# Performance work log

Measured on AMD Instinct MI355X. Metric: run time of the kernel, lower is better.

## Reference

```python
import jax, jax.numpy as jnp
import numpy as np

N, E, G = 200000, 800000, 8192
IN, H, D, EXTRA = 128, 4, 64, 16


def setup_inputs() -> dict:
    key = jax.random.key(0)
    ks = jax.random.split(key, 24)
    inp = {
        'feats_node': jax.random.normal(ks[0], (N, IN), jnp.float32),
        'feats_graph': jax.random.normal(ks[1], (G, EXTRA), jnp.float32),
        'src': jax.random.randint(ks[2], (E,), 0, N, jnp.int32),
        'dst': jax.random.randint(ks[3], (E,), 0, N, jnp.int32),
        'graph_ids': jnp.sort(jax.random.randint(ks[4], (N,), 0, G, jnp.int32)),
        # GAT layer 1: fc [H*D, IN], attn [H, D], bias zeros (DGL default)
        'fc1_w': 0.5 * jax.random.normal(ks[5], (H * D, IN), jnp.float32),
        'attn_l1': 0.5 * jax.random.normal(ks[6], (H, D), jnp.float32),
        'attn_r1': 0.5 * jax.random.normal(ks[7], (H, D), jnp.float32),
        'bias1': jnp.zeros((H * D,), jnp.float32),
        # GAT layer 2
        'fc2_w': 0.5 * jax.random.normal(ks[8], (H * D, H * D), jnp.float32),
        'attn_l2': 0.5 * jax.random.normal(ks[9], (H, D), jnp.float32),
        'attn_r2': 0.5 * jax.random.normal(ks[10], (H, D), jnp.float32),
        'bias2': jnp.zeros((H * D,), jnp.float32),
        # GAT layer 3: 1 head
        'fc3_w': 0.5 * jax.random.normal(ks[11], (D, H * D), jnp.float32),
        'attn_l3': 0.5 * jax.random.normal(ks[12], (1, D), jnp.float32),
        'attn_r3': 0.5 * jax.random.normal(ks[13], (1, D), jnp.float32),
        'bias3': jnp.zeros((D,), jnp.float32),
        # readout score
        'score_w': 0.5 * jax.random.normal(ks[14], (1, D), jnp.float32),
        'score_b': jnp.zeros((1,), jnp.float32),
        # MLP: [D+EXTRA -> 2D -> D -> 1]
        'mlp_w1': 0.5 * jax.random.normal(ks[15], (2 * D, D + EXTRA), jnp.float32),
        'mlp_b1': jnp.zeros((2 * D,), jnp.float32),
        'mlp_w2': 0.5 * jax.random.normal(ks[16], (D, 2 * D), jnp.float32),
        'mlp_b2': jnp.zeros((D,), jnp.float32),
        'mlp_w3': 0.5 * jax.random.normal(ks[17], (1, D), jnp.float32),
        'mlp_b3': jnp.zeros((1,), jnp.float32),
    }
    return inp


def gat_conv(x, src, dst, fc_w, attn_l, attn_r, bias, n_heads, out_dim):
    # DGL GATConv: proj -> edge leaky_relu attention -> per-dst softmax -> aggregate
    n = x.shape[0]
    feat = (x @ fc_w.T).reshape(n, n_heads, out_dim)          # [N,H,D]
    el = jnp.einsum('nhd,hd->nh', feat, attn_l)               # [N,H]
    er = jnp.einsum('nhd,hd->nh', feat, attn_r)
    e = jax.nn.leaky_relu(el[src] + er[dst], 0.2)             # [E,H]
    m = jax.ops.segment_max(e, dst, num_segments=n)           # per-dst max
    m = jax.lax.stop_gradient(jnp.where(jnp.isfinite(m), m, 0.0))
    a = jnp.exp(e - m[dst])                                   # [E,H]
    denom = jax.ops.segment_sum(a, dst, num_segments=n)       # [N,H]
    alpha = a / jnp.where(denom[dst] == 0, 1.0, denom[dst])
    out = jax.ops.segment_sum(alpha[:, :, None] * feat[src], dst, num_segments=n)
    return out + bias.reshape(1, n_heads, out_dim)            # [N,H,D]


def reference(feats_node, feats_graph, src, dst, graph_ids,
              fc1_w, attn_l1, attn_r1, bias1,
              fc2_w, attn_l2, attn_r2, bias2,
              fc3_w, attn_l3, attn_r3, bias3,
              score_w, score_b,
              mlp_w1, mlp_b1, mlp_w2, mlp_b2, mlp_w3, mlp_b3):
    n = feats_node.shape[0]
    g = feats_graph.shape[0]
    x = jax.nn.selu(gat_conv(feats_node, src, dst, fc1_w, attn_l1, attn_r1, bias1, H, D)).reshape(n, H * D)
    x = jax.nn.selu(gat_conv(x, src, dst, fc2_w, attn_l2, attn_r2, bias2, H, D)).reshape(n, H * D)
    x = jax.nn.selu(gat_conv(x, src, dst, fc3_w, attn_l3, attn_r3, bias3, 1, D)).reshape(n, D)
    # weighted-average readout: sum(w*x)/sum(w) per graph
    w = jax.nn.sigmoid(x @ score_w.T + score_b)               # [N,1]
    num = jax.ops.segment_sum(w * x, graph_ids, num_segments=g)
    den = jax.ops.segment_sum(w, graph_ids, num_segments=g)
    emb = num / jnp.where(den == 0, 1.0, den)                 # [G,D]
    z = jnp.concatenate([emb, feats_graph], axis=1)           # [G,D+EXTRA]
    h = jax.nn.selu(z @ mlp_w1.T + mlp_b1)
    h = jax.nn.selu(h @ mlp_w2.T + mlp_b2)
    return h @ mlp_w3.T + mlp_b3                              # [G,1]
```

## Files before the change

### kernel.cpp

```cpp
#include <hip/hip_runtime.h>
#include <math.h>

#define N_NODES 200000
#define N_EDGES 800000
#define N_GRAPHS 8192
#define B1 16
#define B2G 16
#define EC2 128

typedef unsigned short ushort_t;

__device__ __forceinline__ float selu_f(float x){
  const float alpha = 1.6732632423543772f;
  const float lam   = 1.0507009873554805f;
  return x > 0.f ? lam * x : lam * alpha * (expf(x) - 1.f);
}
__device__ __forceinline__ float dot4(float4 a, float4 b){
  return a.x * b.x + a.y * b.y + a.z * b.z + a.w * b.w;
}

__global__ void zero_i32(int* p, int n){
  int i = blockIdx.x * 256 + threadIdx.x;
  if (i < n) p[i] = 0;
}

__global__ void deg_kernel(const int* __restrict__ dst, int* __restrict__ deg, int E){
  int e = blockIdx.x * 256 + threadIdx.x;
  if (e < E) atomicAdd(&deg[dst[e]], 1);
}

__global__ void scan1(const int* __restrict__ deg, int* __restrict__ rp, int* __restrict__ bs, int n){
  __shared__ int sh[256];
  int t = threadIdx.x;
  int base = blockIdx.x * 1024;
  int v[4]; int s = 0;
  #pragma unroll
  for (int i = 0; i < 4; i++){
    int idx = base + t * 4 + i;
    v[i] = (idx < n) ? deg[idx] : 0;
    s += v[i];
  }
  sh[t] = s; __syncthreads();
  for (int off = 1; off < 256; off <<= 1){
    int x = (t >= off) ? sh[t - off] : 0;
    __syncthreads();
    sh[t] += x;
    __syncthreads();
  }
  int run = (t == 0) ? 0 : sh[t - 1];
  #pragma unroll
  for (int i = 0; i < 4; i++){
    int idx = base + t * 4 + i;
    if (idx < n) rp[idx] = run;
    run += v[i];
  }
  if (t == 255) bs[blockIdx.x] = sh[255];
}

__global__ void scan2(int* bs, int nb){
  __shared__ int sh[256];
  int t = threadIdx.x;
  sh[t] = (t < nb) ? bs[t] : 0; __syncthreads();
  for (int off = 1; off < 256; off <<= 1){
    int x = (t >= off) ? sh[t - off] : 0;
    __syncthreads();
    sh[t] += x;
    __syncthreads();
  }
  int excl = (t == 0) ? 0 : sh[t - 1];
  if (t < nb) bs[t] = excl;
}

__global__ void scan3(int* rp, const int* __restrict__ bs, int n, int total){
  int i = blockIdx.x * 256 + threadIdx.x;
  if (i < n) rp[i] += bs[i >> 10];
  if (i == 0) rp[n] = total;
}

__global__ void fill_csr(const int* __restrict__ src, const int* __restrict__ dst,
                         const int* __restrict__ rp, int* __restrict__ fil,
                         int* __restrict__ csr, int E){
  int e = blockIdx.x * 256 + threadIdx.x;
  if (e < E){
    int d = dst[e];
    int p = atomicAdd(&fil[d], 1);
    csr[rp[d] + p] = src[e];
  }
}

__global__ void compute_v(const float* __restrict__ W1, const float* __restrict__ al1, const float* __restrict__ ar1,
                          const float* __restrict__ W2, const float* __restrict__ al2, const float* __restrict__ ar2,
                          const float* __restrict__ W3, const float* __restrict__ al3, const float* __restrict__ ar3,
                          float* __restrict__ V1L, float* __restrict__ V1R,
                          float* __restrict__ V2L, float* __restrict__ V2R,
                          float* __restrict__ V3L, float* __restrict__ V3R){
  int i = blockIdx.x * 256 + threadIdx.x;
  if (i < 512){
    int h = i >> 7, k = i & 127;
    float sl = 0.f, sr = 0.f;
    for (int dd = 0; dd < 64; dd++){
      float w = W1[(size_t)(h * 64 + dd) * 128 + k];
      sl += al1[h * 64 + dd] * w;
      sr += ar1[h * 64 + dd] * w;
    }
    V1L[i] = sl; V1R[i] = sr;
  } else if (i < 1536){
    int j = i - 512;
    int h = j >> 8, k = j & 255;
    float sl = 0.f, sr = 0.f;
    for (int dd = 0; dd < 64; dd++){
      float w = W2[(size_t)(h * 64 + dd) * 256 + k];
      sl += al2[h * 64 + dd] * w;
      sr += ar2[h * 64 + dd] * w;
    }
    V2L[j] = sl; V2R[j] = sr;
  } else if (i < 1792){
    int k = i - 1536;
    float sl = 0.f, sr = 0.f;
    for (int dd = 0; dd < 64; dd++){
      float w = W3[(size_t)dd * 256 + k];
      sl += al3[dd] * w;
      sr += ar3[dd] * w;
    }
    V3L[k] = sl; V3R[k] = sr;
  }
}

__global__ __launch_bounds__(256) void el_er1(const float* __restrict__ x0,
                                              const float* __restrict__ V1L, const float* __restrict__ V1R,
                                              float* __restrict__ el1, float* __restrict__ er1, int n){
  __shared__ float vl[512], vr[512];
  int t = threadIdx.x;
  for (int i = t; i < 512; i += 256){ vl[i] = V1L[i]; vr[i] = V1R[i]; }
  __syncthreads();
  int node = blockIdx.x * 4 + (t >> 6);
  int l = t & 63;
  if (node >= n) return;
  float xa = x0[(size_t)node * 128 + l];
  float xb = x0[(size_t)node * 128 + 64 + l];
  #pragma unroll
  for (int h = 0; h < 4; h++){
    float pl = xa * vl[h * 128 + l] + xb * vl[h * 128 + 64 + l];
    float pr = xa * vr[h * 128 + l] + xb * vr[h * 128 + 64 + l];
    #pragma unroll
    for (int off = 32; off; off >>= 1){ pl += __shfl_xor(pl, off); pr += __shfl_xor(pr, off); }
    if (l == 0){ el1[(size_t)node * 4 + h] = pl; er1[(size_t)node * 4 + h] = pr; }
  }
}

__global__ __launch_bounds__(256) void alpha_h4(const float* __restrict__ el, const float* __restrict__ er,
                                                const int* __restrict__ rp, const int* __restrict__ csr,
                                                float* __restrict__ a, int n){
  int node = blockIdx.x * 256 + threadIdx.x;
  if (node >= n) return;
  int s0 = rp[node], s1 = rp[node + 1];
  if (s0 >= s1) return;
  float4 erv = *reinterpret_cast<const float4*>(er + (size_t)node * 4);
  float m0 = -1e30f, m1 = -1e30f, m2 = -1e30f, m3 = -1e30f;
  for (int i = s0; i < s1; i++){
    float4 e = *reinterpret_cast<const float4*>(el + (size_t)csr[i] * 4);
    float e0 = e.x + erv.x; e0 = e0 > 0.f ? e0 : 0.2f * e0; m0 = fmaxf(m0, e0);
    float e1 = e.y + erv.y; e1 = e1 > 0.f ? e1 : 0.2f * e1; m1 = fmaxf(m1, e1);
    float e2 = e.z + erv.z; e2 = e2 > 0.f ? e2 : 0.2f * e2; m2 = fmaxf(m2, e2);
    float e3 = e.w + erv.w; e3 = e3 > 0.f ? e3 : 0.2f * e3; m3 = fmaxf(m3, e3);
  }
  float d0 = 0.f, d1 = 0.f, d2 = 0.f, d3 = 0.f;
  for (int i = s0; i < s1; i++){
    float4 e = *reinterpret_cast<const float4*>(el + (size_t)csr[i] * 4);
    float e0 = e.x + erv.x; e0 = e0 > 0.f ? e0 : 0.2f * e0; d0 += expf(e0 - m0);
    float e1 = e.y + erv.y; e1 = e1 > 0.f ? e1 : 0.2f * e1; d1 += expf(e1 - m1);
    float e2 = e.z + erv.z; e2 = e2 > 0.f ? e2 : 0.2f * e2; d2 += expf(e2 - m2);
    float e3 = e.w + erv.w; e3 = e3 > 0.f ? e3 : 0.2f * e3; d3 += expf(e3 - m3);
  }
  d0 = 1.f / d0; d1 = 1.f / d1; d2 = 1.f / d2; d3 = 1.f / d3;
  for (int i = s0; i < s1; i++){
    float4 e = *reinterpret_cast<const float4*>(el + (size_t)csr[i] * 4);
    float4 o;
    float e0 = e.x + erv.x; e0 = e0 > 0.f ? e0 : 0.2f * e0; o.x = expf(e0 - m0) * d0;
    float e1 = e.y + erv.y; e1 = e1 > 0.f ? e1 : 0.2f * e1; o.y = expf(e1 - m1) * d1;
    float e2 = e.z + erv.z; e2 = e2 > 0.f ? e2 : 0.2f * e2; o.z = expf(e2 - m2) * d2;
    float e3 = e.w + erv.w; e3 = e3 > 0.f ? e3 : 0.2f * e3; o.w = expf(e3 - m3) * d3;
    *reinterpret_cast<float4*>(a + (size_t)i * 4) = o;
  }
}

__global__ __launch_bounds__(256) void alpha_h1(const float* __restrict__ el, const float* __restrict__ er,
                                                const int* __restrict__ rp, const int* __restrict__ csr,
                                                float* __restrict__ a, int n){
  int node = blockIdx.x * 256 + threadIdx.x;
  if (node >= n) return;
  int s0 = rp[node], s1 = rp[node + 1];
  if (s0 >= s1) return;
  float erv = er[node];
  float m = -1e30f;
  for (int i = s0; i < s1; i++){
    float e = el[csr[i]] + erv; e = e > 0.f ? e : 0.2f * e; m = fmaxf(m, e);
  }
  float den = 0.f;
  for (int i = s0; i < s1; i++){
    float e = el[csr[i]] + erv; e = e > 0.f ? e : 0.2f * e; den += expf(e - m);
  }
  float inv = 1.f / den;
  for (int i = s0; i < s1; i++){
    float e = el[csr[i]] + erv; e = e > 0.f ? e : 0.2f * e; a[i] = expf(e - m) * inv;
  }
}

__global__ __launch_bounds__(512, 4) void l1_fused(
    const float* __restrict__ x0, const float* __restrict__ W1, const float* __restrict__ bias1,
    const float* __restrict__ a1, const float* __restrict__ W2,
    const float* __restrict__ V2L, const float* __restrict__ V2R,
    const int* __restrict__ rp, const int* __restrict__ csr,
    ushort_t* __restrict__ y1hi, unsigned char* __restrict__ y1lo,
    float* __restrict__ el2, float* __restrict__ er2){
  __shared__ float aggT[4][B1][132];
  __shared__ int rpc[B1 + 1];
  float* x1s = &aggT[0][0][0];
  int t = threadIdx.x;
  int nb0 = blockIdx.x * B1;
  if (t <= B1) rpc[t] = rp[nb0 + t];
  __syncthreads();

  {
    int g = t >> 5, c4 = t & 31;
    int i0 = rpc[g], i1 = rpc[g + 1];
    float acc[4][4] = {{0.f}};
    int s = (i0 < i1) ? csr[i0] : 0;
    for (int i = i0; i < i1; i++){
      int sn = (i + 1 < i1) ? csr[i + 1] : 0;
      float4 av = *reinterpret_cast<const float4*>(a1 + (size_t)i * 4);
      float4 xv = *reinterpret_cast<const float4*>(x0 + (size_t)s * 128 + c4 * 4);
      acc[0][0] += av.x * xv.x; acc[0][1] += av.x * xv.y; acc[0][2] += av.x * xv.z; acc[0][3] += av.x * xv.w;
      acc[1][0] += av.y * xv.x; acc[1][1] += av.y * xv.y; acc[1][2] += av.y * xv.z; acc[1][3] += av.y * xv.w;
      acc[2][0] += av.z * xv.x; acc[2][1] += av.z * xv.y; acc[2][2] += av.z * xv.z; acc[2][3] += av.z * xv.w;
      acc[3][0] += av.w * xv.x; acc[3][1] += av.w * xv.y; acc[3][2] += av.w * xv.z; acc[3][3] += av.w * xv.w;
      s = sn;
    }
    #pragma unroll
    for (int h = 0; h < 4; h++){
      float4 v = make_float4(acc[h][0], acc[h][1], acc[h][2], acc[h][3]);
      *reinterpret_cast<float4*>(&aggT[h][g][c4 * 4]) = v;
    }
  }
  __syncthreads();

  float r1[8];
  {
    int m = t & 255, dq = t >> 8;
    int h = m >> 6;
    #pragma unroll
    for (int r = 0; r < 8; r++) r1[r] = 0.f;
    const float* wp = W1 + (size_t)m * 128;
    #pragma unroll 4
    for (int kq = 0; kq < 32; kq++){
      float4 w = *reinterpret_cast<const float4*>(wp + kq * 4);
      #pragma unroll
      for (int r = 0; r < 8; r++){
        float4 a = *reinterpret_cast<const float4*>(&aggT[h][dq * 8 + r][kq * 4]);
        r1[r] += dot4(w, a);
      }
    }
  }
  __syncthreads();
  {
    int m = t & 255, dq = t >> 8;
    float b = bias1[m];
    #pragma unroll
    for (int r = 0; r < 8; r++)
      x1s[(dq * 8 + r) * 260 + m] = selu_f(r1[r] + b);
  }
  __syncthreads();

  {
    int m = t & 255, dq = t >> 8;
    float acc[8];
    #pragma unroll
    for (int r = 0; r < 8; r++) acc[r] = 0.f;
    const float* wp = W2 + (size_t)m * 256;
    #pragma unroll 4
    for (int kq = 0; kq < 64; kq++){
      float4 w = *reinterpret_cast<const float4*>(wp + kq * 4);
      #pragma unroll
      for (int r = 0; r < 8; r++){
        float4 xv = *reinterpret_cast<const float4*>(&x1s[(dq * 8 + r) * 260 + kq * 4]);
        acc[r] += dot4(w, xv);
      }
    }
    #pragma unroll
    for (int r = 0; r < 8; r++){
      int d = dq * 8 + r;
      unsigned int u = __float_as_uint(acc[r]);
      u += 0x80u;
      y1hi[(size_t)(nb0 + d) * 256 + m] = (ushort_t)(u >> 16);
      y1lo[(size_t)(nb0 + d) * 256 + m] = (unsigned char)(u >> 8);
    }
  }

  if (t < 128){
    int d = t & 15, hq = (t >> 4) & 3, lr = t >> 6;
    const float* V = lr ? V2R : V2L;
    const float4* Vq = reinterpret_cast<const float4*>(V + hq * 256);
    const float4* Xq = reinterpret_cast<const float4*>(&x1s[d * 260]);
    float p = 0.f;
    #pragma unroll 4
    for (int q = 0; q < 64; q++){
      float4 v = Vq[q]; float4 x = Xq[q];
      p += v.x * x.x; p += v.y * x.y; p += v.z * x.z; p += v.w * x.w;
    }
    if (lr) er2[(size_t)(nb0 + d) * 4 + hq] = p;
    else    el2[(size_t)(nb0 + d) * 4 + hq] = p;
  }
}

__global__ __launch_bounds__(256, 4) void l2_gather(
    const ushort_t* __restrict__ y1hi, const unsigned char* __restrict__ y1lo,
    const float* __restrict__ bias2, const float* __restrict__ a2,
    const float* __restrict__ W3,
    const float* __restrict__ V3L, const float* __restrict__ V3R,
    const int* __restrict__ rp, const int* __restrict__ csr,
    float* __restrict__ feat3, float* __restrict__ el3, float* __restrict__ er3){
  __shared__ float x2s[B2G][257];
  __shared__ float W3c[16 * 257];
  __shared__ float als[EC2][4];
  __shared__ int   ssrc[EC2];
  __shared__ int   rpc[B2G + 1];
  int t = threadIdx.x;
  int nb0 = blockIdx.x * B2G;
  if (t <= B2G) rpc[t] = rp[nb0 + t];
  __syncthreads();
  int e0 = rpc[0], eN = rpc[B2G];
  int c = t;
  int h = c >> 6;

  float acc[B2G];
  #pragma unroll
  for (int d = 0; d < B2G; d++) acc[d] = 0.f;

  for (int c0 = e0; c0 < eN; c0 += EC2){
    int ce = min(EC2, eN - c0);
    for (int i = t; i < ce; i += 256){
      ssrc[i] = csr[c0 + i];
      float4 av = *reinterpret_cast<const float4*>(a2 + (size_t)(c0 + i) * 4);
      als[i][0] = av.x; als[i][1] = av.y; als[i][2] = av.z; als[i][3] = av.w;
    }
    __syncthreads();
    #pragma unroll
    for (int d = 0; d < B2G; d++){
      int lo = max(rpc[d], c0) - c0;
      int hi = min(rpc[d + 1], c0 + ce) - c0;
      for (int i = lo; i < hi; i++){
        size_t s = (size_t)ssrc[i] * 256 + c;
        unsigned int u = ((unsigned int)y1hi[s] << 16) | ((unsigned int)y1lo[s] << 8);
        acc[d] += als[i][h] * __uint_as_float(u);
      }
    }
    __syncthreads();
  }
  {
    float b = bias2[c];
    #pragma unroll
    for (int d = 0; d < B2G; d++) x2s[d][c] = selu_f(acc[d] + b);
  }
  __syncthreads();

  {
    int task = t >> 3, j = t & 7;
    int d = task & 15, lr = task >> 4;
    const float* V = lr ? V3R : V3L;
    float p = 0.f;
    for (int kk = 0; kk < 32; kk++){
      int k = j + kk * 8;
      p += V[k] * x2s[d][k];
    }
    p += __shfl_xor(p, 1); p += __shfl_xor(p, 2); p += __shfl_xor(p, 4);
    if (j == 0){ if (lr) er3[nb0 + d] = p; else el3[nb0 + d] = p; }
  }

  for (int ch = 0; ch < 4; ch++){
    __syncthreads();
    for (int i = t; i < 16 * 64; i += 256){
      int r = i >> 6, k4 = i & 63;
      float4 w = *reinterpret_cast<const float4*>(W3 + (size_t)(ch * 16 + r) * 256 + k4 * 4);
      W3c[r * 257 + k4 * 4 + 0] = w.x; W3c[r * 257 + k4 * 4 + 1] = w.y;
      W3c[r * 257 + k4 * 4 + 2] = w.z; W3c[r * 257 + k4 * 4 + 3] = w.w;
    }
    __syncthreads();
    {
      int r = t & 15, d = t >> 4;
      float s = 0.f;
      #pragma unroll 4
      for (int k = 0; k < 256; k++) s += W3c[r * 257 + k] * x2s[d][k];
      feat3[(size_t)(nb0 + d) * 64 + ch * 16 + r] = s;
    }
  }
}

__global__ __launch_bounds__(256) void gat_agg3(const float* __restrict__ feat, const float* __restrict__ a3,
                                                const int* __restrict__ rp, const int* __restrict__ csr,
                                                const float* __restrict__ bias,
                                                float* __restrict__ out, int n){
  int node = blockIdx.x * 4 + (threadIdx.x >> 6);
  int t = threadIdx.x & 63;
  if (node >= n) return;
  int s0 = rp[node], s1 = rp[node + 1];
  float acc = 0.f;
  for (int i = s0; i < s1; i += 4){
    float a[4], f[4];
    #pragma unroll
    for (int j = 0; j < 4; j++){
      int idx = i + j;
      bool vld = idx < s1;
      int idc = vld ? idx : s1 - 1;
      float av = a3[idc];
      if (!vld) av = 0.f;
      a[j] = av;
      f[j] = feat[(size_t)csr[idc] * 64 + t];
    }
    acc += a[0] * f[0] + a[1] * f[1] + a[2] * f[2] + a[3] * f[3];
  }
  out[(size_t)node * 64 + t] = selu_f(acc + bias[t]);
}

__global__ void readout_kernel(const float* __restrict__ x3, const float* __restrict__ score_w,
                               const float* __restrict__ score_b, const int* __restrict__ gids,
                               float* __restrict__ num, float* __restrict__ den, int n){
  int node = blockIdx.x * 4 + (threadIdx.x >> 6);
  int lane = threadIdx.x & 63;
  if (node >= n) return;
  float xv = x3[(size_t)node * 64 + lane];
  float p = xv * score_w[lane];
  #pragma unroll
  for (int off = 32; off; off >>= 1) p += __shfl_xor(p, off);
  float w = 1.f / (1.f + expf(-(p + score_b[0])));
  int g = gids[node];
  atomicAdd(&num[(size_t)g * 64 + lane], w * xv);
  if (lane == 0) atomicAdd(&den[g], w);
}

__global__ __launch_bounds__(128) void mlp_kernel(
    const float* __restrict__ num, const float* __restrict__ den,
    const float* __restrict__ fg,
    const float* __restrict__ w1, const float* __restrict__ b1,
    const float* __restrict__ w2, const float* __restrict__ b2,
    const float* __restrict__ w3, const float* __restrict__ b3,
    float* __restrict__ out, int G){
  __shared__ float z[80];
  __shared__ float h1[128];
  __shared__ float h2[64];
  int t = threadIdx.x;
  for (int g = blockIdx.x; g < G; g += gridDim.x){
    if (t < 64){
      float d = den[g];
      d = (d == 0.f) ? 1.f : d;
      z[t] = num[(size_t)g * 64 + t] / d;
    } else if (t < 80){
      z[t] = fg[(size_t)g * 16 + (t - 64)];
    }
    __syncthreads();
    {
      float a = b1[t];
      for (int k = 0; k < 80; k++) a += z[k] * w1[t * 80 + k];
      h1[t] = selu_f(a);
    }
    __syncthreads();
    if (t < 64){
      float a = b2[t];
      for (int k = 0; k < 128; k++) a += h1[k] * w2[t * 128 + k];
      h2[t] = selu_f(a);
    }
    __syncthreads();
    if (t < 64){
      float p = h2[t] * w3[t];
      #pragma unroll
      for (int off = 32; off; off >>= 1) p += __shfl_down(p, off);
      if (t == 0) out[g] = p + b3[0];
    }
    __syncthreads();
  }
}

extern "C" void kernel_launch(void* const* d_in, const int* in_sizes, int n_in,
                              void* d_out, int out_size, void* d_ws, size_t ws_size,
                              hipStream_t stream) {
  const float* feats_node  = (const float*)d_in[0];
  const float* feats_graph = (const float*)d_in[1];
  const int*   src         = (const int*)d_in[2];
  const int*   dst         = (const int*)d_in[3];
  const int*   gids        = (const int*)d_in[4];
  const float* fc1_w   = (const float*)d_in[5];
  const float* attn_l1 = (const float*)d_in[6];
  const float* attn_r1 = (const float*)d_in[7];
  const float* bias1   = (const float*)d_in[8];
  const float* fc2_w   = (const float*)d_in[9];
  const float* attn_l2 = (const float*)d_in[10];
  const float* attn_r2 = (const float*)d_in[11];
  const float* bias2   = (const float*)d_in[12];
  const float* fc3_w   = (const float*)d_in[13];
  const float* attn_l3 = (const float*)d_in[14];
  const float* attn_r3 = (const float*)d_in[15];
  const float* bias3   = (const float*)d_in[16];
  const float* score_w = (const float*)d_in[17];
  const float* score_b = (const float*)d_in[18];
  const float* mlp_w1  = (const float*)d_in[19];
  const float* mlp_b1  = (const float*)d_in[20];
  const float* mlp_w2  = (const float*)d_in[21];
  const float* mlp_b2  = (const float*)d_in[22];
  const float* mlp_w3  = (const float*)d_in[23];
  const float* mlp_b3  = (const float*)d_in[24];
  float* out = (float*)d_out;

  char* ws = (char*)d_ws;
  size_t off = 0;
  auto alloc = [&](size_t bytes) -> void* {
    void* p = ws + off;
    off += (bytes + 255) / 256 * 256;
    return p;
  };
  int*   deg   = (int*)alloc((size_t)N_NODES * 4);
  int*   fil   = (int*)alloc((size_t)N_NODES * 4);
  int*   rp    = (int*)alloc((size_t)(N_NODES + 1) * 4);
  int*   bs    = (int*)alloc(256 * 4);
  int*   csr   = (int*)alloc((size_t)N_EDGES * 4);
  float* elbuf = (float*)alloc((size_t)N_NODES * 4 * 4);
  float* erbuf = (float*)alloc((size_t)N_NODES * 4 * 4);
  float* V1L   = (float*)alloc(512 * 4);
  float* V1R   = (float*)alloc(512 * 4);
  float* V2L   = (float*)alloc(1024 * 4);
  float* V2R   = (float*)alloc(1024 * 4);
  float* V3L   = (float*)alloc(256 * 4);
  float* V3R   = (float*)alloc(256 * 4);
  float* num   = (float*)alloc((size_t)N_GRAPHS * 64 * 4);
  float* den   = (float*)alloc((size_t)N_GRAPHS * 4);
  float* A     = (float*)alloc((size_t)N_EDGES * 4 * 4);
  float* feat3 = (float*)alloc((size_t)N_NODES * 64 * 4);
  ushort_t*      y1hi = (ushort_t*)alloc((size_t)N_NODES * 256 * 2);
  unsigned char* y1lo = (unsigned char*)alloc((size_t)N_NODES * 256);
  float* x3 = (float*)y1hi;

  zero_i32<<<(N_NODES + 255) / 256, 256, 0, stream>>>(deg, N_NODES);
  zero_i32<<<(N_NODES + 255) / 256, 256, 0, stream>>>(fil, N_NODES);
  zero_i32<<<(N_GRAPHS * 64 + 255) / 256, 256, 0, stream>>>((int*)num, N_GRAPHS * 64);
  zero_i32<<<(N_GRAPHS + 255) / 256, 256, 0, stream>>>((int*)den, N_GRAPHS);

  deg_kernel<<<(N_EDGES + 255) / 256, 256, 0, stream>>>(dst, deg, N_EDGES);
  scan1<<<196, 256, 0, stream>>>(deg, rp, bs, N_NODES);
  scan2<<<1, 256, 0, stream>>>(bs, 196);
  scan3<<<(N_NODES + 255) / 256, 256, 0, stream>>>(rp, bs, N_NODES, N_EDGES);
  fill_csr<<<(N_EDGES + 255) / 256, 256, 0, stream>>>(src, dst, rp, fil, csr, N_EDGES);

  compute_v<<<7, 256, 0, stream>>>(fc1_w, attn_l1, attn_r1, fc2_w, attn_l2, attn_r2,
                                   fc3_w, attn_l3, attn_r3, V1L, V1R, V2L, V2R, V3L, V3R);
  el_er1<<<N_NODES / 4, 256, 0, stream>>>(feats_node, V1L, V1R, elbuf, erbuf, N_NODES);

  alpha_h4<<<(N_NODES + 255) / 256, 256, 0, stream>>>(elbuf, erbuf, rp, csr, A, N_NODES);
  l1_fused<<<N_NODES / B1, 512, 0, stream>>>(feats_node, fc1_w, bias1, A, fc2_w,
                                             V2L, V2R, rp, csr, y1hi, y1lo, elbuf, erbuf);
  alpha_h4<<<(N_NODES + 255) / 256, 256, 0, stream>>>(elbuf, erbuf, rp, csr, A, N_NODES);
  l2_gather<<<N_NODES / B2G, 256, 0, stream>>>(y1hi, y1lo, bias2, A, fc3_w,
                                               V3L, V3R, rp, csr, feat3, elbuf, erbuf);
  alpha_h1<<<(N_NODES + 255) / 256, 256, 0, stream>>>(elbuf, erbuf, rp, csr, A, N_NODES);
  gat_agg3<<<N_NODES / 4, 256, 0, stream>>>(feat3, A, rp, csr, bias3, x3, N_NODES);

  readout_kernel<<<N_NODES / 4, 256, 0, stream>>>(x3, score_w, score_b, gids, num, den, N_NODES);
  mlp_kernel<<<256, 128, 0, stream>>>(num, den, feats_graph,
                                      mlp_w1, mlp_b1, mlp_w2, mlp_b2, mlp_w3, mlp_b3,
                                      out, N_GRAPHS);
}
```

Baseline: 2.430 ms.

## Double layer-1 node block and register-tile the fused GEMMs 4x4 per thread

Layer-1 fused kernel now processes 32 nodes per block instead of 16. The gather phase uses 16 threads per node with 8 columns each. Both dense projections (W1 and W2) now compute a 4-output by 4-node register tile per thread, so each weight load is reused across more nodes and each shared-memory read feeds four outputs. The packed hi/lo stores are vectorized. The aggT shared array is enlarged to hold x1s for 32 rows, which raises shared-memory use and register pressure and may reduce occupancy.

```diff
diff --git a/kernel.cpp b/kernel.cpp
--- a/kernel.cpp
+++ b/kernel.cpp
@@ -4,7 +4,7 @@
 #define N_NODES 200000
 #define N_EDGES 800000
 #define N_GRAPHS 8192
-#define B1 16
+#define B1 32
 #define B2G 16
 #define EC2 128
 
@@ -213,7 +213,7 @@
     const int* __restrict__ rp, const int* __restrict__ csr,
     ushort_t* __restrict__ y1hi, unsigned char* __restrict__ y1lo,
     float* __restrict__ el2, float* __restrict__ er2){
-  __shared__ float aggT[4][B1][132];
+  __shared__ float aggT[4][33][132];
   __shared__ int rpc[B1 + 1];
   float* x1s = &aggT[0][0][0];
   int t = threadIdx.x;
@@ -222,82 +222,124 @@
   __syncthreads();
 
   {
-    int g = t >> 5, c4 = t & 31;
+    int g = t >> 4, c8 = t & 15;
     int i0 = rpc[g], i1 = rpc[g + 1];
-    float acc[4][4] = {{0.f}};
+    float acc[4][8] = {{0.f}};
     int s = (i0 < i1) ? csr[i0] : 0;
     for (int i = i0; i < i1; i++){
       int sn = (i + 1 < i1) ? csr[i + 1] : 0;
       float4 av = *reinterpret_cast<const float4*>(a1 + (size_t)i * 4);
-      float4 xv = *reinterpret_cast<const float4*>(x0 + (size_t)s * 128 + c4 * 4);
-      acc[0][0] += av.x * xv.x; acc[0][1] += av.x * xv.y; acc[0][2] += av.x * xv.z; acc[0][3] += av.x * xv.w;
-      acc[1][0] += av.y * xv.x; acc[1][1] += av.y * xv.y; acc[1][2] += av.y * xv.z; acc[1][3] += av.y * xv.w;
-      acc[2][0] += av.z * xv.x; acc[2][1] += av.z * xv.y; acc[2][2] += av.z * xv.z; acc[2][3] += av.z * xv.w;
-      acc[3][0] += av.w * xv.x; acc[3][1] += av.w * xv.y; acc[3][2] += av.w * xv.z; acc[3][3] += av.w * xv.w;
+      float4 xa = *reinterpret_cast<const float4*>(x0 + (size_t)s * 128 + c8 * 8);
+      float4 xb = *reinterpret_cast<const float4*>(x0 + (size_t)s * 128 + c8 * 8 + 4);
+      acc[0][0] += av.x * xa.x; acc[0][1] += av.x * xa.y; acc[0][2] += av.x * xa.z; acc[0][3] += av.x * xa.w;
+      acc[0][4] += av.x * xb.x; acc[0][5] += av.x * xb.y; acc[0][6] += av.x * xb.z; acc[0][7] += av.x * xb.w;
+      acc[1][0] += av.y * xa.x; acc[1][1] += av.y * xa.y; acc[1][2] += av.y * xa.z; acc[1][3] += av.y * xa.w;
+      acc[1][4] += av.y * xb.x; acc[1][5] += av.y * xb.y; acc[1][6] += av.y * xb.z; acc[1][7] += av.y * xb.w;
+      acc[2][0] += av.z * xa.x; acc[2][1] += av.z * xa.y; acc[2][2] += av.z * xa.z; acc[2][3] += av.z * xa.w;
+      acc[2][4] += av.z * xb.x; acc[2][5] += av.z * xb.y; acc[2][6] += av.z * xb.z; acc[2][7] += av.z * xb.w;
+      acc[3][0] += av.w * xa.x; acc[3][1] += av.w * xa.y; acc[3][2] += av.w * xa.z; acc[3][3] += av.w * xa.w;
+      acc[3][4] += av.w * xb.x; acc[3][5] += av.w * xb.y; acc[3][6] += av.w * xb.z; acc[3][7] += av.w * xb.w;
       s = sn;
     }
     #pragma unroll
     for (int h = 0; h < 4; h++){
-      float4 v = make_float4(acc[h][0], acc[h][1], acc[h][2], acc[h][3]);
-      *reinterpret_cast<float4*>(&aggT[h][g][c4 * 4]) = v;
+      float4 v0 = make_float4(acc[h][0], acc[h][1], acc[h][2], acc[h][3]);
+      float4 v1 = make_float4(acc[h][4], acc[h][5], acc[h][6], acc[h][7]);
+      *reinterpret_cast<float4*>(&aggT[h][g][c8 * 8]) = v0;
+      *reinterpret_cast<float4*>(&aggT[h][g][c8 * 8 + 4]) = v1;
     }
   }
   __syncthreads();
 
-  float r1[8];
+  int wv = t >> 6, ln = t & 63;
+  int hh = wv & 3;
+  int mq = hh * 16 + (ln & 15);
+  int dg = (wv >> 2) * 4 + (ln >> 4);
+  int m0 = mq * 4;
+
+  float acc1[4][4];
   {
-    int m = t & 255, dq = t >> 8;
-    int h = m >> 6;
-    #pragma unroll
-    for (int r = 0; r < 8; r++) r1[r] = 0.f;
-    const float* wp = W1 + (size_t)m * 128;
-    #pragma unroll 4
+    #pragma unroll
+    for (int j = 0; j < 4; j++)
+      #pragma unroll
+      for (int r = 0; r < 4; r++) acc1[j][r] = 0.f;
+    const float* wp = W1 + (size_t)m0 * 128;
+    #pragma unroll 2
     for (int kq = 0; kq < 32; kq++){
-      float4 w = *reinterpret_cast<const float4*>(wp + kq * 4);
+      int k = kq * 4;
+      float4 w0 = *reinterpret_cast<const float4*>(wp + k);
+      float4 w1 = *reinterpret_cast<const float4*>(wp + 128 + k);
+      float4 w2 = *reinterpret_cast<const float4*>(wp + 256 + k);
+      float4 w3 = *reinterpret_cast<const float4*>(wp + 384 + k);
       #pragma unroll
-      for (int r = 0; r < 8; r++){
-        float4 a = *reinterpret_cast<const float4*>(&aggT[h][dq * 8 + r][kq * 4]);
-        r1[r] += dot4(w, a);
+      for (int r = 0; r < 4; r++){
+        float4 a = *reinterpret_cast<const float4*>(&aggT[hh][dg + 8 * r][k]);
+        acc1[0][r] += dot4(w0, a);
+        acc1[1][r] += dot4(w1, a);
+        acc1[2][r] += dot4(w2, a);
+        acc1[3][r] += dot4(w3, a);
       }
     }
   }
   __syncthreads();
   {
-    int m = t & 255, dq = t >> 8;
-    float b = bias1[m];
-    #pragma unroll
-    for (int r = 0; r < 8; r++)
-      x1s[(dq * 8 + r) * 260 + m] = selu_f(r1[r] + b);
+    float4 b = *reinterpret_cast<const float4*>(bias1 + m0);
+    #pragma unroll
+    for (int r = 0; r < 4; r++){
+      int d = dg + 8 * r;
+      float4 v;
+      v.x = selu_f(acc1[0][r] + b.x);
+      v.y = selu_f(acc1[1][r] + b.y);
+      v.z = selu_f(acc1[2][r] + b.z);
+      v.w = selu_f(acc1[3][r] + b.w);
+      *reinterpret_cast<float4*>(&x1s[d * 260 + m0]) = v;
+    }
   }
   __syncthreads();
 
   {
-    int m = t & 255, dq = t >> 8;
-    float acc[8];
-    #pragma unroll
-    for (int r = 0; r < 8; r++) acc[r] = 0.f;
-    const float* wp = W2 + (size_t)m * 256;
-    #pragma unroll 4
+    float acc2[4][4];
+    #pragma unroll
+    for (int j = 0; j < 4; j++)
+      #pragma unroll
+      for (int r = 0; r < 4; r++) acc2[j][r] = 0.f;
+    const float* wp = W2 + (size_t)m0 * 256;
+    #pragma unroll 2
     for (int kq = 0; kq < 64; kq++){
-      float4 w = *reinterpret_cast<const float4*>(wp + kq * 4);
+      int k = kq * 4;
+      float4 w0 = *reinterpret_cast<const float4*>(wp + k);
+      float4 w1 = *reinterpret_cast<const float4*>(wp + 256 + k);
+      float4 w2 = *reinterpret_cast<const float4*>(wp + 512 + k);
+      float4 w3 = *reinterpret_cast<const float4*>(wp + 768 + k);
       #pragma unroll
-      for (int r = 0; r < 8; r++){
-        float4 xv = *reinterpret_cast<const float4*>(&x1s[(dq * 8 + r) * 260 + kq * 4]);
-        acc[r] += dot4(w, xv);
+      for (int r = 0; r < 4; r++){
+        float4 xv = *reinterpret_cast<const float4*>(&x1s[(dg + 8 * r) * 260 + k]);
+        acc2[0][r] += dot4(w0, xv);
+        acc2[1][r] += dot4(w1, xv);
+        acc2[2][r] += dot4(w2, xv);
+        acc2[3][r] += dot4(w3, xv);
       }
     }
     #pragma unroll
-    for (int r = 0; r < 8; r++){
-      int d = dq * 8 + r;
-      unsigned int u = __float_as_uint(acc[r]);
-      u += 0x80u;
-      y1hi[(size_t)(nb0 + d) * 256 + m] = (ushort_t)(u >> 16);
-      y1lo[(size_t)(nb0 + d) * 256 + m] = (unsigned char)(u >> 8);
-    }
-  }
-
-  if (t < 128){
-    int d = t & 15, hq = (t >> 4) & 3, lr = t >> 6;
+    for (int r = 0; r < 4; r++){
+      int d = dg + 8 * r;
+      unsigned int u0 = __float_as_uint(acc2[0][r]) + 0x80u;
+      unsigned int u1 = __float_as_uint(acc2[1][r]) + 0x80u;
+      unsigned int u2 = __float_as_uint(acc2[2][r]) + 0x80u;
+      unsigned int u3 = __float_as_uint(acc2[3][r]) + 0x80u;
+      ushort4 h4; uchar4 l4;
+      h4.x = (ushort_t)(u0 >> 16); h4.y = (ushort_t)(u1 >> 16);
+      h4.z = (ushort_t)(u2 >> 16); h4.w = (ushort_t)(u3 >> 16);
+      l4.x = (unsigned char)(u0 >> 8); l4.y = (unsigned char)(u1 >> 8);
+      l4.z = (unsigned char)(u2 >> 8); l4.w = (unsigned char)(u3 >> 8);
+      size_t base = (size_t)(nb0 + d) * 256 + m0;
+      *reinterpret_cast<ushort4*>(y1hi + base) = h4;
+      *reinterpret_cast<uchar4*>(y1lo + base) = l4;
+    }
+  }
+
+  if (t < 256){
+    int d = t & 31, hq = (t >> 5) & 3, lr = t >> 7;
     const float* V = lr ? V2R : V2L;
     const float4* Vq = reinterpret_cast<const float4*>(V + hq * 256);
     const float4* Xq = reinterpret_cast<const float4*>(&x1s[d * 260]);
```

Result: slower. 3.424 ms (+40.9%).
